# Kernel tuning notes

Measured on AMD Instinct MI355X. Metric: run time of the kernel, lower is better.

## Reference

```python
import jax, jax.numpy as jnp
import numpy as np

EPS = 1e-8

def _matrix_sqrt(cov):
    # e @ diag(max(w,EPS))**0.5 @ e.T
    w, e = jnp.linalg.eigh(cov)
    w = jnp.maximum(w, EPS)
    return (e * jnp.sqrt(w)[None, :]) @ e.T

def _matrix_sqrt_neg(cov):
    # cov jittered on diagonal, then e @ diag(1/max(w,EPS))**0.5 @ e.T
    D = cov.shape[-1]
    cov = cov * (jnp.ones_like(cov) + jnp.eye(D, dtype=cov.dtype) * 0.001)
    w, e = jnp.linalg.eigh(cov)
    w = jnp.maximum(w, EPS)
    return (e * (1.0 / jnp.sqrt(w))[None, :]) @ e.T

def _match_axis(xc, R, mu, counter):
    # xc: (C, M, D) per-channel rows; R: (C, D, D) accumulated second moment; mu: (C, D)
    mu_test = xc.mean(1, keepdims=True)                      # (C,1,D)
    h = xc - mu_test                                         # centered test features
    cov_train = R / counter - mu[:, :, None] * mu[:, None, :]  # (C,D,D)
    sqrt_train = jax.vmap(_matrix_sqrt)(cov_train)           # (C,D,D)
    M = h.shape[1]
    cov_test = jnp.einsum('cmd,cme->cde', h, h) / M          # (C,D,D)
    neg_sqrt_test = jax.vmap(_matrix_sqrt_neg)(cov_test)     # (C,D,D)
    T = jnp.einsum('cde,cef->cdf', neg_sqrt_test, sqrt_train)  # whiten-then-recolor map
    return jnp.einsum('cmd,cdf->cmf', h, T) + mu[:, None, :]

def reference(x, cov_H, mu_H, cov_W, mu_W, counter):
    N, H, W, C = x.shape
    cnt = jnp.asarray(counter, dtype=x.dtype)
    # H-axis matching: rows of length H, per channel
    xh = x.transpose(3, 0, 2, 1).reshape(C, N * W, H)
    xh = _match_axis(xh, cov_H, mu_H, cnt)
    # W-axis matching: rows of length W, per channel
    xw = xh.reshape(C, N, W, H).transpose(0, 1, 3, 2).reshape(C, N * H, W)
    xw = _match_axis(xw, cov_W, mu_W, cnt)
    return xw.reshape(C, N, H, W).transpose(1, 2, 3, 0)

def setup_inputs() -> dict:
    key = jax.random.key(0)
    k1, k2, k3, k4, k5 = jax.random.split(key, 5)
    N, H, W, C = 64, 56, 56, 256
    counter = 716800  # accumulated sample count (N*W per acc batch)
    x = jax.random.normal(k1, (N, H, W, C), dtype=jnp.float32)
    mu_H = 0.1 * jax.random.normal(k2, (C, H), dtype=jnp.float32)
    mu_W = 0.1 * jax.random.normal(k3, (C, W), dtype=jnp.float32)
    # Build accumulated second moments so R/counter - outer(mu) is PSD
    BH = jax.random.normal(k4, (C, H, H), dtype=jnp.float32)
    SH = jnp.einsum('cij,ckj->cik', BH, BH) / H + 0.1 * jnp.eye(H, dtype=jnp.float32)
    cov_H = (SH + mu_H[:, :, None] * mu_H[:, None, :]) * counter
    BW = jax.random.normal(k5, (C, W, W), dtype=jnp.float32)
    SW = jnp.einsum('cij,ckj->cik', BW, BW) / W + 0.1 * jnp.eye(W, dtype=jnp.float32)
    cov_W = (SW + mu_W[:, :, None] * mu_W[:, None, :]) * counter
    return {"x": x, "cov_H": cov_H, "mu_H": mu_H, "cov_W": cov_W, "mu_W": mu_W, "counter": counter}
```

## Files before the change

kernel.cpp:

```cpp
#include <hip/hip_runtime.h>

#define C_ 256
#define D_ 56
#define N_ 64
#define M_ 3584
#define DD_ 3136
#define PL_ 200704
#define NS_ITERS 16

typedef __attribute__((ext_vector_type(8))) short v8s;
typedef __attribute__((ext_vector_type(8))) _Float16 v8h;
typedef __attribute__((ext_vector_type(4))) _Float16 v4h;
typedef __attribute__((ext_vector_type(4))) float v4f;

__device__ __forceinline__ unsigned short f2bf(float f) {
  union { float f; unsigned u; } x; x.f = f;
  unsigned r = x.u + 0x7FFFu + ((x.u >> 16) & 1u);
  return (unsigned short)(r >> 16);
}
__device__ __forceinline__ float bf2f(unsigned short h) {
  union { unsigned u; float f; } x; x.u = ((unsigned)h) << 16;
  return x.f;
}

__global__ __launch_bounds__(256) void k_tin(const float* __restrict__ x, _Float16* __restrict__ A) {
  int b = blockIdx.x;
  int cchunk = b & 3, g = b >> 2;
  int c0 = cchunk * 64;
  int m0 = g * 4;
  int n = m0 / 56, w0 = m0 % 56;
  __shared__ _Float16 t[4][56][66];
  int tid = threadIdx.x;
  const float4* x4 = (const float4*)x;
  #pragma unroll
  for (int it = 0; it < 14; ++it) {
    int i = tid + 256*it;
    int mloc = i / 896, r = i % 896;
    int h = r >> 4, cg = r & 15;
    float4 v = x4[((size_t)n*3136 + (size_t)h*56 + (w0+mloc))*64 + (c0>>2) + cg];
    t[mloc][h][4*cg+0] = (_Float16)v.x;
    t[mloc][h][4*cg+1] = (_Float16)v.y;
    t[mloc][h][4*cg+2] = (_Float16)v.z;
    t[mloc][h][4*cg+3] = (_Float16)v.w;
  }
  __syncthreads();
  #pragma unroll
  for (int it = 0; it < 7; ++it) {
    int j = tid + 256*it;
    int q = j / 7, hg = j % 7;
    int cc = q >> 2, mloc = q & 3;
    v8h o;
    #pragma unroll
    for (int k = 0; k < 8; ++k) o[k] = t[mloc][hg*8+k][cc];
    *(v8h*)&A[(size_t)(c0+cc)*PL_ + (size_t)(m0+mloc)*56 + hg*8] = o;
  }
}

__device__ __forceinline__ void mm_split_h(const _Float16 (*Ah)[72], const _Float16 (*Al)[72],
                                           const _Float16 (*Bh)[72], const _Float16 (*Bl)[72],
                                           int w, int lr, int lq, v4f (&acc)[4]) {
  v8h ah[2], al[2], bh[4][2], bl[4][2];
  #pragma unroll
  for (int s = 0; s < 2; ++s) {
    int kb = 32*s + 8*lq;
    ah[s] = *(const v8h*)&Ah[16*w + lr][kb];
    al[s] = *(const v8h*)&Al[16*w + lr][kb];
    #pragma unroll
    for (int jt = 0; jt < 4; ++jt) {
      bh[jt][s] = *(const v8h*)&Bh[16*jt + lr][kb];
      bl[jt][s] = *(const v8h*)&Bl[16*jt + lr][kb];
    }
  }
  #pragma unroll
  for (int jt = 0; jt < 4; ++jt) {
    #pragma unroll
    for (int s = 0; s < 2; ++s) {
      acc[jt] = __builtin_amdgcn_mfma_f32_16x16x32_f16(ah[s], bh[jt][s], acc[jt], 0, 0, 0);
      acc[jt] = __builtin_amdgcn_mfma_f32_16x16x32_f16(ah[s], bl[jt][s], acc[jt], 0, 0, 0);
      acc[jt] = __builtin_amdgcn_mfma_f32_16x16x32_f16(al[s], bh[jt][s], acc[jt], 0, 0, 0);
    }
  }
}

__device__ __forceinline__ void store_split_h(_Float16 (*H)[72], _Float16 (*L)[72],
                                              int w, int lr, int lq, const v4f (&val)[4]) {
  #pragma unroll
  for (int jt = 0; jt < 4; ++jt) {
    #pragma unroll
    for (int e = 0; e < 4; ++e) {
      int i = 16*w + 4*lq + e, j = 16*jt + lr;
      float v = val[jt][e];
      _Float16 h = (_Float16)v;
      H[i][j] = h;
      L[i][j] = (_Float16)(v - (float)h);
    }
  }
}

__global__ __launch_bounds__(256) void k_stats(const _Float16* __restrict__ in,
                                               float* __restrict__ muPart,
                                               float* __restrict__ covPart) {
  int b = blockIdx.x;
  int c = b >> 3, s = b & 7;
  const _Float16* p = in + (size_t)c*PL_ + (size_t)(s*448)*56;
  __shared__ __align__(16) char lds[18432];
  unsigned short (*At)[72]  = (unsigned short(*)[72])lds;
  unsigned short (*Alt)[72] = (unsigned short(*)[72])(lds + 9216);
  float (*Qbuf)[66] = (float(*)[66])lds;
  float (*red2)[60] = (float(*)[60])lds;
  int tid = threadIdx.x;
  int cg = tid % 7, rg = tid / 7;
  bool act = tid < 224;
  float cs[8] = {0.f,0.f,0.f,0.f,0.f,0.f,0.f,0.f};

  int l = tid & 63, w = tid >> 6;
  int lr = l & 15, lq = l >> 4;
  v4f zero4 = {0.f, 0.f, 0.f, 0.f};
  v4f accP[4], accQ[4];
  #pragma unroll
  for (int j = 0; j < 4; ++j) { accP[j] = zero4; accQ[j] = zero4; }

  for (int ch = 0; ch < 7; ++ch) {
    __syncthreads();
    if (act) {
      #pragma unroll
      for (int u = 0; u < 2; ++u) {
        int m = rg + 32*u;
        v8h v = *(const v8h*)&p[(size_t)(ch*64 + m)*56 + cg*8];
        #pragma unroll
        for (int k = 0; k < 8; ++k) {
          float f = (float)v[k];
          cs[k] += f;
          unsigned short h = f2bf(f);
          At[cg*8+k][m] = h;
          Alt[cg*8+k][m] = f2bf(f - bf2f(h));
        }
      }
    }
    __syncthreads();
    #pragma unroll
    for (int s2 = 0; s2 < 2; ++s2) {
      int kb = 32*s2 + 8*lq;
      v8s a = *(const v8s*)&At[16*w + lr][kb];
      #pragma unroll
      for (int j = 0; j < 4; ++j) {
        v8s bh = *(const v8s*)&At[16*j + lr][kb];
        v8s bl = *(const v8s*)&Alt[16*j + lr][kb];
        accP[j] = __builtin_amdgcn_mfma_f32_16x16x32_bf16(a, bh, accP[j], 0, 0, 0);
        accQ[j] = __builtin_amdgcn_mfma_f32_16x16x32_bf16(a, bl, accQ[j], 0, 0, 0);
      }
    }
  }

  __syncthreads();
  if (act) {
    #pragma unroll
    for (int k = 0; k < 8; ++k) red2[rg][cg*8+k] = cs[k];
  }
  __syncthreads();
  if (tid < 64) {
    float m = 0.f;
    if (tid < 56) {
      #pragma unroll
      for (int r = 0; r < 32; ++r) m += red2[r][tid];
    }
    muPart[((size_t)s*C_ + c)*64 + tid] = m;
  }
  __syncthreads();

  #pragma unroll
  for (int j = 0; j < 4; ++j) {
    #pragma unroll
    for (int e = 0; e < 4; ++e) {
      int r = 16*w + 4*lq + e, cc = 16*j + lr;
      Qbuf[r][cc] = accQ[j][e];
    }
  }
  __syncthreads();
  float* op = covPart + ((size_t)s*C_ + c)*DD_;
  #pragma unroll
  for (int j = 0; j < 4; ++j) {
    #pragma unroll
    for (int e = 0; e < 4; ++e) {
      int r = 16*w + 4*lq + e, cc = 16*j + lr;
      if (r < 56 && cc < 56) op[r*56 + cc] = accP[j][e] + accQ[j][e] + Qbuf[cc][r];
    }
  }
}

__global__ __launch_bounds__(256) void k_mured(const float* __restrict__ muPart, float* __restrict__ muT) {
  int idx = blockIdx.x*256 + threadIdx.x;
  if (idx >= C_*64) return;
  int c = idx >> 6, lane = idx & 63;
  float s = 0.f;
  for (int p = 0; p < 8; ++p) s += muPart[((size_t)p*C_ + c)*64 + lane];
  muT[idx] = s * (1.0f/M_);
}

__global__ __launch_bounds__(256) void k_finalize(const float* __restrict__ covPart, const float* __restrict__ muT,
                                                  const float* __restrict__ covIn, const float* __restrict__ muTrn,
                                                  const int* __restrict__ counter,
                                                  float* __restrict__ covTest, float* __restrict__ covTr) {
  int idx = blockIdx.x*256 + threadIdx.x;
  const int total = C_*DD_;
  if (idx < total) {
    int c = idx / DD_, r2 = idx % DD_, i = r2/56, j = r2%56;
    float ssum = 0.f;
    for (int s = 0; s < 8; ++s) ssum += covPart[((size_t)s*C_ + c)*DD_ + r2];
    float v = ssum*(1.0f/M_) - muT[c*64+i]*muT[c*64+j];
    if (i == j) v *= 1.001f;
    covTest[idx] = v;
  } else if (idx < 2*total) {
    int k = idx - total;
    int c = k / DD_, r2 = k % DD_, i = r2/56, j = r2%56;
    float cnt = (float)counter[0];
    covTr[k] = covIn[k]/cnt - muTrn[c*56+i]*muTrn[c*56+j];
  }
}

__global__ __launch_bounds__(256) void k_ns(const float* __restrict__ covTr, const float* __restrict__ covTest,
                                            float* __restrict__ Sout, float* __restrict__ Zout) {
  __shared__ __align__(16) _Float16 mats[6][64][72];
  __shared__ float red[4];
  int tid = threadIdx.x;
  int which = blockIdx.x & 1, c = blockIdx.x >> 1;
  const float4* Ain4 = (const float4*)((which ? covTest : covTr) + (size_t)c * DD_);

  typedef _Float16 (*mat_t)[72];
  mat_t Yh = mats[0], Yl = mats[1], Zh = mats[2], Zl = mats[3], Th = mats[4], Tl = mats[5];

  float ss = 0.f;
  for (int i4 = tid; i4 < 784; i4 += 256) {
    float4 v = Ain4[i4];
    ss += v.x*v.x + v.y*v.y + v.z*v.z + v.w*v.w;
  }
  { unsigned* z = (unsigned*)mats; for (int i = tid; i < 13824; i += 256) z[i] = 0u; }
  #pragma unroll
  for (int off = 32; off > 0; off >>= 1) ss += __shfl_down(ss, off, 64);
  if ((tid & 63) == 0) red[tid >> 6] = ss;
  __syncthreads();
  float s = sqrtf(red[0] + red[1] + red[2] + red[3]);
  float inv = 1.f / s;

  for (int i4 = tid; i4 < 784; i4 += 256) {
    float4 v = Ain4[i4];
    int r = i4 / 14, cgx = (i4 % 14) * 4;
    float f0 = v.x*inv, f1 = v.y*inv, f2 = v.z*inv, f3 = v.w*inv;
    v4h hh, ll;
    hh.x = (_Float16)f0; ll.x = (_Float16)(f0 - (float)hh.x);
    hh.y = (_Float16)f1; ll.y = (_Float16)(f1 - (float)hh.y);
    hh.z = (_Float16)f2; ll.z = (_Float16)(f2 - (float)hh.z);
    hh.w = (_Float16)f3; ll.w = (_Float16)(f3 - (float)hh.w);
    *(v4h*)&Yh[r][cgx] = hh;
    *(v4h*)&Yl[r][cgx] = ll;
  }
  if (tid < 56) Zh[tid][tid] = (_Float16)1.0f;
  __syncthreads();

  int lane = tid & 63, w = tid >> 6, lr = lane & 15, lq = lane >> 4;
  v4f zero4 = {0.f, 0.f, 0.f, 0.f};
  float rs = sqrtf(s);
  float fac = which ? (1.f/rs) : rs;
  float* outp = (which ? Zout : Sout) + (size_t)c*DD_;

  for (int it = 0; it < NS_ITERS; ++it) {
    v4f accW[4] = {zero4, zero4, zero4, zero4};
    mm_split_h(Zh, Zl, Yh, Yl, w, lr, lq, accW);
    v4f Tv[4];
    #pragma unroll
    for (int jt = 0; jt < 4; ++jt) {
      #pragma unroll
      for (int e = 0; e < 4; ++e) {
        float dv = (16*w + 4*lq + e == 16*jt + lr) ? 1.5f : 0.f;
        Tv[jt][e] = dv - 0.5f*accW[jt][e];
      }
    }
    store_split_h(Th, Tl, w, lr, lq, Tv);
    __syncthreads();
    if (it == NS_ITERS - 1) {
      v4f accF[4] = {zero4, zero4, zero4, zero4};
      if (which == 0) mm_split_h(Yh, Yl, Th, Tl, w, lr, lq, accF);
      else            mm_split_h(Th, Tl, Zh, Zl, w, lr, lq, accF);
      #pragma unroll
      for (int jt = 0; jt < 4; ++jt) {
        #pragma unroll
        for (int e = 0; e < 4; ++e) {
          int i = 16*w + 4*lq + e, j = 16*jt + lr;
          if (i < 56 && j < 56) outp[i*56 + j] = accF[jt][e] * fac;
        }
      }
    } else {
      v4f accY[4] = {zero4, zero4, zero4, zero4};
      v4f accZ[4] = {zero4, zero4, zero4, zero4};
      mm_split_h(Yh, Yl, Th, Tl, w, lr, lq, accY);
      mm_split_h(Th, Tl, Zh, Zl, w, lr, lq, accZ);
      __syncthreads();
      store_split_h(Yh, Yl, w, lr, lq, accY);
      store_split_h(Zh, Zl, w, lr, lq, accZ);
      __syncthreads();
    }
  }
}

__global__ __launch_bounds__(256) void k_tmap(const float* __restrict__ Zi, const float* __restrict__ Sm,
                                              float* __restrict__ Tm) {
  __shared__ __align__(16) _Float16 mats[4][64][72];
  int c = blockIdx.x, tid = threadIdx.x;
  typedef _Float16 (*mat_t)[72];
  mat_t Ah = mats[0], Al = mats[1], Bh = mats[2], Bl = mats[3];
  { unsigned* z = (unsigned*)mats; for (int i = tid; i < 9216; i += 256) z[i] = 0u; }
  __syncthreads();
  const float4* Z4 = (const float4*)(Zi + (size_t)c*DD_);
  const float4* S4 = (const float4*)(Sm + (size_t)c*DD_);
  for (int i4 = tid; i4 < 784; i4 += 256) {
    int r = i4 / 14, cgx = (i4 % 14) * 4;
    float4 v = Z4[i4];
    v4h hh, ll;
    hh.x = (_Float16)v.x; ll.x = (_Float16)(v.x - (float)hh.x);
    hh.y = (_Float16)v.y; ll.y = (_Float16)(v.y - (float)hh.y);
    hh.z = (_Float16)v.z; ll.z = (_Float16)(v.z - (float)hh.z);
    hh.w = (_Float16)v.w; ll.w = (_Float16)(v.w - (float)hh.w);
    *(v4h*)&Ah[r][cgx] = hh;
    *(v4h*)&Al[r][cgx] = ll;
    v = S4[i4];
    hh.x = (_Float16)v.x; ll.x = (_Float16)(v.x - (float)hh.x);
    hh.y = (_Float16)v.y; ll.y = (_Float16)(v.y - (float)hh.y);
    hh.z = (_Float16)v.z; ll.z = (_Float16)(v.z - (float)hh.z);
    hh.w = (_Float16)v.w; ll.w = (_Float16)(v.w - (float)hh.w);
    *(v4h*)&Bh[r][cgx] = hh;
    *(v4h*)&Bl[r][cgx] = ll;
  }
  __syncthreads();
  int lane = tid & 63, w = tid >> 6, lr = lane & 15, lq = lane >> 4;
  v4f zero4 = {0.f, 0.f, 0.f, 0.f};
  v4f acc[4] = {zero4, zero4, zero4, zero4};
  mm_split_h(Ah, Al, Bh, Bl, w, lr, lq, acc);
  float* op = Tm + (size_t)c*DD_;
  #pragma unroll
  for (int jt = 0; jt < 4; ++jt) {
    #pragma unroll
    for (int e = 0; e < 4; ++e) {
      int i = 16*w + 4*lq + e, j = 16*jt + lr;
      if (i < 56 && j < 56) op[i*56 + j] = acc[jt][e];
    }
  }
}

__global__ __launch_bounds__(256) void k_apply(const _Float16* __restrict__ in, const float* __restrict__ muT,
                                               const float* __restrict__ Tmp, const float* __restrict__ muTrain,
                                               _Float16* __restrict__ out, int stage) {
  int b = blockIdx.x;
  int c = b >> 6, n = b & 63;
  __shared__ __align__(16) char lds[18432];
  _Float16 (*Abf)[72] = (_Float16(*)[72])lds;
  _Float16 (*Tt)[72]  = (_Float16(*)[72])(lds + 9216);
  float (*Y)[67] = (float(*)[67])lds;
  __shared__ float smu[64], smt[64];
  int tid = threadIdx.x;
  if (tid < 64) {
    smu[tid] = muT[c*64 + tid];
    smt[tid] = (tid < 56) ? muTrain[c*56 + tid] : 0.f;
  }
  if (tid < 128) {
    int row = tid & 63;
    _Float16 (*Mz)[72] = (tid < 64) ? Abf : Tt;
    *(float4*)&Mz[row][56] = make_float4(0.f, 0.f, 0.f, 0.f);
  }
  __syncthreads();
  const v8h* p8 = (const v8h*)(in + (size_t)c*PL_ + (size_t)n*3136);
  const float4* t4 = (const float4*)(Tmp + (size_t)c*DD_);
  for (int i = tid; i < 392; i += 256) {
    int row = i / 7, cg = i % 7;
    v8h v = p8[row*7 + cg];
    v8h pk;
    #pragma unroll
    for (int k = 0; k < 8; ++k) pk[k] = (_Float16)((float)v[k] - smu[cg*8+k]);
    *(v8h*)&Abf[row][cg*8] = pk;
  }
  for (int i = tid; i < 784; i += 256) {
    float4 t = t4[i];
    int row = i / 14, cgx = (i % 14) * 4;
    Tt[cgx+0][row] = (_Float16)t.x;
    Tt[cgx+1][row] = (_Float16)t.y;
    Tt[cgx+2][row] = (_Float16)t.z;
    Tt[cgx+3][row] = (_Float16)t.w;
  }
  __syncthreads();
  int l = tid & 63, w = tid >> 6;
  int lr = l & 15, lq = l >> 4;
  v4f zero4 = {0.f, 0.f, 0.f, 0.f};
  v4f acc[4];
  #pragma unroll
  for (int j = 0; j < 4; ++j) acc[j] = zero4;
  #pragma unroll
  for (int s = 0; s < 2; ++s) {
    int kb = 32*s + 8*lq;
    v8h a = *(const v8h*)&Abf[16*w + lr][kb];
    #pragma unroll
    for (int j = 0; j < 4; ++j) {
      v8h bb = *(const v8h*)&Tt[16*j + lr][kb];
      acc[j] = __builtin_amdgcn_mfma_f32_16x16x32_f16(a, bb, acc[j], 0, 0, 0);
    }
  }
  __syncthreads();
  #pragma unroll
  for (int j = 0; j < 4; ++j) {
    #pragma unroll
    for (int e = 0; e < 4; ++e) {
      int r = 16*w + 4*lq + e, cc = 16*j + lr;
      Y[r][cc] = acc[j][e] + smt[cc];
    }
  }
  __syncthreads();
  _Float16* o16 = out + (size_t)c*PL_ + (size_t)n*3136;
  if (stage == 1) {
    for (int i = tid; i < 392; i += 256) {
      int h = i / 7, wg = i % 7;
      v8h o;
      #pragma unroll
      for (int k = 0; k < 8; ++k) o[k] = (_Float16)Y[wg*8+k][h];
      *(v8h*)&o16[h*56 + wg*8] = o;
    }
  } else {
    for (int i = tid; i < 392; i += 256) {
      int h = i / 7, wg = i % 7;
      v8h o;
      #pragma unroll
      for (int k = 0; k < 8; ++k) o[k] = (_Float16)Y[h][wg*8+k];
      *(v8h*)&o16[h*56 + wg*8] = o;
    }
  }
}

__global__ __launch_bounds__(256) void k_tout(const _Float16* __restrict__ A2, float* __restrict__ out) {
  int b = blockIdx.x;
  int cchunk = b & 3, g = b >> 2;
  int c0 = cchunk * 64;
  int nh0 = g * 4;
  __shared__ _Float16 t[4][56][66];
  int tid = threadIdx.x;
  #pragma unroll
  for (int it = 0; it < 7; ++it) {
    int j = tid + 256*it;
    int q = j / 7, wg = j % 7;
    int cc = q >> 2, mloc = q & 3;
    v8h v = *(const v8h*)&A2[(size_t)(c0+cc)*PL_ + (size_t)(nh0+mloc)*56 + wg*8];
    #pragma unroll
    for (int k = 0; k < 8; ++k) t[mloc][wg*8+k][cc] = v[k];
  }
  __syncthreads();
  float4* o4 = (float4*)out;
  #pragma unroll
  for (int it = 0; it < 14; ++it) {
    int i = tid + 256*it;
    int mloc = i / 896, r = i % 896;
    int w = r >> 4, cg = r & 15;
    float4 o;
    o.x = (float)t[mloc][w][4*cg+0];
    o.y = (float)t[mloc][w][4*cg+1];
    o.z = (float)t[mloc][w][4*cg+2];
    o.w = (float)t[mloc][w][4*cg+3];
    o4[((size_t)(nh0+mloc)*56 + w)*64 + (c0>>2) + cg] = o;
  }
}

extern "C" void kernel_launch(void* const* d_in, const int* in_sizes, int n_in,
                              void* d_out, int out_size, void* d_ws, size_t ws_size,
                              hipStream_t stream) {
  (void)in_sizes; (void)n_in; (void)out_size;
  const float* x    = (const float*)d_in[0];
  const float* covH = (const float*)d_in[1];
  const float* muH  = (const float*)d_in[2];
  const float* covW = (const float*)d_in[3];
  const float* muW  = (const float*)d_in[4];
  const int*   cnt  = (const int*)d_in[5];
  float* out = (float*)d_out;

  char* ws = (char*)d_ws;
  size_t off = 0;
  auto allocB = [&](size_t nbytes) {
    void* p = ws + off;
    off += ((nbytes + 255) / 256) * 256;
    return p;
  };
  _Float16* A16a  = (_Float16*)allocB((size_t)C_ * PL_ * 2);
  _Float16* A16b  = (_Float16*)allocB((size_t)C_ * PL_ * 2);
  float* covPart  = (float*)allocB((size_t)8 * C_ * DD_ * 4);
  float* muPart   = (float*)allocB((size_t)8 * C_ * 64 * 4);
  float* covTest  = (float*)allocB((size_t)C_ * DD_ * 4);
  float* covTr    = (float*)allocB((size_t)C_ * DD_ * 4);
  float* Sm       = (float*)allocB((size_t)C_ * DD_ * 4);
  float* Zim      = (float*)allocB((size_t)C_ * DD_ * 4);
  float* Tm       = (float*)allocB((size_t)C_ * DD_ * 4);
  float* muT      = (float*)allocB((size_t)C_ * 64 * 4);
  if (off > ws_size) return;

  dim3 blk(256);
  const int finGrid = (2*C_*DD_ + 255)/256;

  k_tin<<<dim3(4 * (M_/4)), blk, 0, stream>>>(x, A16a);

  k_stats   <<<dim3(2048),  blk, 0, stream>>>(A16a, muPart, covPart);
  k_mured   <<<dim3(64),    blk, 0, stream>>>(muPart, muT);
  k_finalize<<<dim3(finGrid), blk, 0, stream>>>(covPart, muT, covH, muH, cnt, covTest, covTr);
  k_ns      <<<dim3(512),   blk, 0, stream>>>(covTr, covTest, Sm, Zim);
  k_tmap    <<<dim3(256),   blk, 0, stream>>>(Zim, Sm, Tm);
  k_apply   <<<dim3(16384), blk, 0, stream>>>(A16a, muT, Tm, muH, A16b, 1);

  k_stats   <<<dim3(2048),  blk, 0, stream>>>(A16b, muPart, covPart);
  k_mured   <<<dim3(64),    blk, 0, stream>>>(muPart, muT);
  k_finalize<<<dim3(finGrid), blk, 0, stream>>>(covPart, muT, covW, muW, cnt, covTest, covTr);
  k_ns      <<<dim3(512),   blk, 0, stream>>>(covTr, covTest, Sm, Zim);
  k_tmap    <<<dim3(256),   blk, 0, stream>>>(Zim, Sm, Tm);
  k_apply   <<<dim3(16384), blk, 0, stream>>>(A16b, muT, Tm, muW, A16a, 2);

  k_tout<<<dim3(4 * (M_/4)), blk, 0, stream>>>(A16a, out);
}
```

Measured before the change: 500.0 us.

## Prefetch next chunk in stats and batch four images per apply block

The stats kernel now loads the next 64-row chunk into registers before the MFMA work on the current chunk, so global latency overlaps compute. The apply kernel now handles four images per block, converting the T matrix to transposed fp16 once and reusing it, and prefetches the next image's input during the current MFMA. This cuts redundant T conversion and launch count, in exchange for fewer blocks, larger LDS (separate Y buffer) and more barriers per block.

```diff
diff --git a/kernel.cpp b/kernel.cpp
--- a/kernel.cpp
+++ b/kernel.cpp
@@ -120,13 +120,18 @@
   #pragma unroll
   for (int j = 0; j < 4; ++j) { accP[j] = zero4; accQ[j] = zero4; }
 
+  v8h pre[2];
+  if (act) {
+    #pragma unroll
+    for (int u = 0; u < 2; ++u)
+      pre[u] = *(const v8h*)&p[(size_t)(rg + 32*u)*56 + cg*8];
+  }
   for (int ch = 0; ch < 7; ++ch) {
-    __syncthreads();
     if (act) {
       #pragma unroll
       for (int u = 0; u < 2; ++u) {
         int m = rg + 32*u;
-        v8h v = *(const v8h*)&p[(size_t)(ch*64 + m)*56 + cg*8];
+        v8h v = pre[u];
         #pragma unroll
         for (int k = 0; k < 8; ++k) {
           float f = (float)v[k];
@@ -138,6 +143,11 @@
       }
     }
     __syncthreads();
+    if (ch < 6 && act) {
+      #pragma unroll
+      for (int u = 0; u < 2; ++u)
+        pre[u] = *(const v8h*)&p[(size_t)((ch+1)*64 + rg + 32*u)*56 + cg*8];
+    }
     #pragma unroll
     for (int s2 = 0; s2 < 2; ++s2) {
       int kb = 32*s2 + 8*lq;
@@ -150,9 +160,9 @@
         accQ[j] = __builtin_amdgcn_mfma_f32_16x16x32_bf16(a, bl, accQ[j], 0, 0, 0);
       }
     }
-  }
-
-  __syncthreads();
+    __syncthreads();
+  }
+
   if (act) {
     #pragma unroll
     for (int k = 0; k < 8; ++k) red2[rg][cg*8+k] = cs[k];
@@ -350,11 +360,11 @@
                                                const float* __restrict__ Tmp, const float* __restrict__ muTrain,
                                                _Float16* __restrict__ out, int stage) {
   int b = blockIdx.x;
-  int c = b >> 6, n = b & 63;
-  __shared__ __align__(16) char lds[18432];
-  _Float16 (*Abf)[72] = (_Float16(*)[72])lds;
-  _Float16 (*Tt)[72]  = (_Float16(*)[72])(lds + 9216);
-  float (*Y)[67] = (float(*)[67])lds;
+  int c = b >> 4, ng = b & 15;
+  int n0 = ng * 4;
+  __shared__ __align__(16) _Float16 Abf[64][72];
+  __shared__ __align__(16) _Float16 Tt[64][72];
+  __shared__ float Y[56][57];
   __shared__ float smu[64], smt[64];
   int tid = threadIdx.x;
   if (tid < 64) {
@@ -366,17 +376,7 @@
     _Float16 (*Mz)[72] = (tid < 64) ? Abf : Tt;
     *(float4*)&Mz[row][56] = make_float4(0.f, 0.f, 0.f, 0.f);
   }
-  __syncthreads();
-  const v8h* p8 = (const v8h*)(in + (size_t)c*PL_ + (size_t)n*3136);
   const float4* t4 = (const float4*)(Tmp + (size_t)c*DD_);
-  for (int i = tid; i < 392; i += 256) {
-    int row = i / 7, cg = i % 7;
-    v8h v = p8[row*7 + cg];
-    v8h pk;
-    #pragma unroll
-    for (int k = 0; k < 8; ++k) pk[k] = (_Float16)((float)v[k] - smu[cg*8+k]);
-    *(v8h*)&Abf[row][cg*8] = pk;
-  }
   for (int i = tid; i < 784; i += 256) {
     float4 t = t4[i];
     int row = i / 14, cgx = (i % 14) * 4;
@@ -385,50 +385,75 @@
     Tt[cgx+2][row] = (_Float16)t.z;
     Tt[cgx+3][row] = (_Float16)t.w;
   }
-  __syncthreads();
   int l = tid & 63, w = tid >> 6;
   int lr = l & 15, lq = l >> 4;
   v4f zero4 = {0.f, 0.f, 0.f, 0.f};
-  v4f acc[4];
-  #pragma unroll
-  for (int j = 0; j < 4; ++j) acc[j] = zero4;
-  #pragma unroll
-  for (int s = 0; s < 2; ++s) {
-    int kb = 32*s + 8*lq;
-    v8h a = *(const v8h*)&Abf[16*w + lr][kb];
+  const v8h* p8base = (const v8h*)(in + (size_t)c*PL_);
+
+  v8h preA[2], preB[2];
+  {
+    const v8h* p8 = p8base + (size_t)n0*392;
+    #pragma unroll
+    for (int u = 0; u < 2; ++u) { int i = tid + 256*u; if (i < 392) preA[u] = p8[i]; }
+  }
+  for (int t = 0; t < 4; ++t) {
+    #pragma unroll
+    for (int u = 0; u < 2; ++u) {
+      int i = tid + 256*u;
+      if (i < 392) {
+        int row = i / 7, cg = i % 7;
+        v8h pk;
+        #pragma unroll
+        for (int k = 0; k < 8; ++k) pk[k] = (_Float16)((float)preA[u][k] - smu[cg*8+k]);
+        *(v8h*)&Abf[row][cg*8] = pk;
+      }
+    }
+    __syncthreads();
+    if (t < 3) {
+      const v8h* p8 = p8base + (size_t)(n0+t+1)*392;
+      #pragma unroll
+      for (int u = 0; u < 2; ++u) { int i = tid + 256*u; if (i < 392) preB[u] = p8[i]; }
+    }
+    v4f acc[4] = {zero4, zero4, zero4, zero4};
+    #pragma unroll
+    for (int s = 0; s < 2; ++s) {
+      int kb = 32*s + 8*lq;
+      v8h a = *(const v8h*)&Abf[16*w + lr][kb];
+      #pragma unroll
+      for (int j = 0; j < 4; ++j) {
+        v8h bb = *(const v8h*)&Tt[16*j + lr][kb];
+        acc[j] = __builtin_amdgcn_mfma_f32_16x16x32_f16(a, bb, acc[j], 0, 0, 0);
+      }
+    }
+    __syncthreads();
     #pragma unroll
     for (int j = 0; j < 4; ++j) {
-      v8h bb = *(const v8h*)&Tt[16*j + lr][kb];
-      acc[j] = __builtin_amdgcn_mfma_f32_16x16x32_f16(a, bb, acc[j], 0, 0, 0);
-    }
-  }
-  __syncthreads();
-  #pragma unroll
-  for (int j = 0; j < 4; ++j) {
-    #pragma unroll
-    for (int e = 0; e < 4; ++e) {
-      int r = 16*w + 4*lq + e, cc = 16*j + lr;
-      Y[r][cc] = acc[j][e] + smt[cc];
-    }
-  }
-  __syncthreads();
-  _Float16* o16 = out + (size_t)c*PL_ + (size_t)n*3136;
-  if (stage == 1) {
-    for (int i = tid; i < 392; i += 256) {
-      int h = i / 7, wg = i % 7;
-      v8h o;
-      #pragma unroll
-      for (int k = 0; k < 8; ++k) o[k] = (_Float16)Y[wg*8+k][h];
-      *(v8h*)&o16[h*56 + wg*8] = o;
-    }
-  } else {
-    for (int i = tid; i < 392; i += 256) {
-      int h = i / 7, wg = i % 7;
-      v8h o;
-      #pragma unroll
-      for (int k = 0; k < 8; ++k) o[k] = (_Float16)Y[h][wg*8+k];
-      *(v8h*)&o16[h*56 + wg*8] = o;
-    }
+      #pragma unroll
+      for (int e = 0; e < 4; ++e) {
+        int r = 16*w + 4*lq + e, cc = 16*j + lr;
+        if (r < 56 && cc < 56) Y[r][cc] = acc[j][e] + smt[cc];
+      }
+    }
+    __syncthreads();
+    _Float16* o16 = out + (size_t)c*PL_ + (size_t)(n0+t)*3136;
+    if (stage == 1) {
+      for (int i = tid; i < 392; i += 256) {
+        int h = i / 7, wg = i % 7;
+        v8h o;
+        #pragma unroll
+        for (int k = 0; k < 8; ++k) o[k] = (_Float16)Y[wg*8+k][h];
+        *(v8h*)&o16[h*56 + wg*8] = o;
+      }
+    } else {
+      for (int i = tid; i < 392; i += 256) {
+        int h = i / 7, wg = i % 7;
+        v8h o;
+        #pragma unroll
+        for (int k = 0; k < 8; ++k) o[k] = (_Float16)Y[h][wg*8+k];
+        *(v8h*)&o16[h*56 + wg*8] = o;
+      }
+    }
+    preA[0] = preB[0]; preA[1] = preB[1];
   }
 }
 
@@ -505,14 +530,14 @@
   k_finalize<<<dim3(finGrid), blk, 0, stream>>>(covPart, muT, covH, muH, cnt, covTest, covTr);
   k_ns      <<<dim3(512),   blk, 0, stream>>>(covTr, covTest, Sm, Zim);
   k_tmap    <<<dim3(256),   blk, 0, stream>>>(Zim, Sm, Tm);
-  k_apply   <<<dim3(16384), blk, 0, stream>>>(A16a, muT, Tm, muH, A16b, 1);
+  k_apply   <<<dim3(4096),  blk, 0, stream>>>(A16a, muT, Tm, muH, A16b, 1);
 
   k_stats   <<<dim3(2048),  blk, 0, stream>>>(A16b, muPart, covPart);
   k_mured   <<<dim3(64),    blk, 0, stream>>>(muPart, muT);
   k_finalize<<<dim3(finGrid), blk, 0, stream>>>(covPart, muT, covW, muW, cnt, covTest, covTr);
   k_ns      <<<dim3(512),   blk, 0, stream>>>(covTr, covTest, Sm, Zim);
   k_tmap    <<<dim3(256),   blk, 0, stream>>>(Zim, Sm, Tm);
-  k_apply   <<<dim3(16384), blk, 0, stream>>>(A16b, muT, Tm, muW, A16a, 2);
+  k_apply   <<<dim3(4096),  blk, 0, stream>>>(A16b, muT, Tm, muW, A16a, 2);
 
   k_tout<<<dim3(4 * (M_/4)), blk, 0, stream>>>(A16a, out);
 }
```

New measurement: 491.4 us. About the same (-1.7%).
